# Performance work log

Hardware: AMD Instinct MI355X
Metric: run time of the kernel (lower is better)

## Reference

```python
import jax, jax.numpy as jnp
import numpy as np

NDIM = 8
P = NDIM * (NDIM - 1) // 2  # 28 upper-triangular pairs
NHIDDEN = 128
NLAYERS = 3  # first layer + (NLAYERS-1) hidden layers, all followed by softplus
BATCH = 65536


def _pair_indices():
    # torch code iterates j outer, i inner, keeping i < j (i >= j skipped)
    pairs = [(i, j) for j in range(NDIM) for i in range(NDIM) if i < j]
    rel = np.array([[k for k in range(NDIM) if k != i and k != j] for (i, j) in pairs],
                   dtype=np.int32)  # [P, NDIM-2]
    i_idx = np.array([p[0] for p in pairs], dtype=np.int32)
    j_idx = np.array([p[1] for p in pairs], dtype=np.int32)
    return rel, i_idx, j_idx


def setup_inputs() -> dict:
    key = jax.random.key(0)
    ks = jax.random.split(key, 7)
    rel, i_idx, j_idx = _pair_indices()
    d_in = NDIM - 2
    x = jax.random.normal(ks[0], (BATCH, NDIM), dtype=jnp.float32)
    # stacked per-pair MLP parameters (kaiming-ish scale)
    W1 = jax.random.normal(ks[1], (P, d_in, NHIDDEN), dtype=jnp.float32) / np.sqrt(d_in)
    b1 = jax.random.normal(ks[2], (P, NHIDDEN), dtype=jnp.float32) * 0.05
    Wh = jax.random.normal(ks[3], (NLAYERS - 1, P, NHIDDEN, NHIDDEN), dtype=jnp.float32) / np.sqrt(NHIDDEN)
    bh = jax.random.normal(ks[4], (NLAYERS - 1, P, NHIDDEN), dtype=jnp.float32) * 0.05
    Wout = jax.random.normal(ks[5], (P, NHIDDEN), dtype=jnp.float32) / np.sqrt(NHIDDEN)
    bout = jax.random.normal(ks[6], (P,), dtype=jnp.float32) * 0.05
    return {
        "x": x, "W1": W1, "b1": b1, "Wh": Wh, "bh": bh,
        "Wout": Wout, "bout": bout,
        "rel_idx": jnp.asarray(rel), "i_idx": jnp.asarray(i_idx), "j_idx": jnp.asarray(j_idx),
    }


def reference(x, W1, b1, Wh, bh, Wout, bout, rel_idx, i_idx, j_idx):
    # gather the ndim-2 relevant coords for every pair: [B, P, NDIM-2]
    xg = x[:, rel_idx]
    # first linear + softplus (batched over the P pairs)
    h = jax.nn.softplus(jnp.einsum('bpd,pdh->bph', xg, W1) + b1)
    # hidden linears + softplus
    for l in range(Wh.shape[0]):
        h = jax.nn.softplus(jnp.einsum('bph,phk->bpk', h, Wh[l]) + bh[l])
    # output head (no activation): scalar per pair -> [B, P]
    vals = jnp.einsum('bph,ph->bp', h, Wout) + bout
    # scatter into upper triangle, then antisymmetrize
    B = x.shape[0]
    J = jnp.zeros((B, NDIM, NDIM), dtype=x.dtype).at[:, i_idx, j_idx].set(vals)
    return J - jnp.swapaxes(J, 1, 2)
```

## Files before the change

### kernel.cpp

```cpp
#include <hip/hip_runtime.h>

#define NDIM 8
#define P_PAIRS 28
#define HID 128
#define BATCH_N 65536
#define TILE_M 256
#define THREADS 1024
#define TILES_PER_BLOCK 4

#define LOG2E 1.4426950408889634f
#define LN2   0.6931471805599453f

typedef __attribute__((ext_vector_type(8))) short bf16x8;
typedef __attribute__((ext_vector_type(4))) float f32x4;

#define MEM_FENCE asm volatile("" ::: "memory")

__device__ __forceinline__ unsigned short f32_to_bf16(float f) {
  union { float f; unsigned u; } v; v.f = f;
  unsigned r = v.u + 0x7FFFu + ((v.u >> 16) & 1u);
  return (unsigned short)(r >> 16);
}

__device__ __forceinline__ unsigned cvt_pk_bf16(float a, float b) {
  unsigned r;
  asm("v_cvt_pk_bf16_f32 %0, %1, %2" : "=v"(r) : "v"(a), "v"(b));
  return r;
}

__device__ __forceinline__ float fast_exp2(float x) {
  float r; asm("v_exp_f32 %0, %1" : "=v"(r) : "v"(x)); return r;
}
__device__ __forceinline__ float fast_log2(float x) {
  float r; asm("v_log_f32 %0, %1" : "=v"(r) : "v"(x)); return r;
}

__device__ __forceinline__ float softplus2(float t) {
  t = fminf(t, 30.0f);
  return fast_log2(1.0f + fast_exp2(t));
}

__device__ __forceinline__ int swz(int r, int c8) {
  return r * 128 + (((c8 ^ (r & 15)) & 15) << 3);
}

__global__ void prep_wt(const float* __restrict__ Wh, unsigned short* __restrict__ WT) {
  __shared__ float tile[32][33];
  int t = blockIdx.x;
  int lp = t >> 4;
  int sub = t & 15;
  int kt = (sub >> 2) * 32, nt = (sub & 3) * 32;
  const float* src = Wh + (size_t)lp * 16384;
  unsigned short* dst = WT + (size_t)lp * 16384;
  int tx = threadIdx.x & 31, ty = threadIdx.x >> 5;
#pragma unroll
  for (int r = 0; r < 32; r += 8)
    tile[r + ty][tx] = src[(kt + r + ty) * 128 + (nt + tx)];
  __syncthreads();
#pragma unroll
  for (int r = 0; r < 32; r += 8)
    dst[(nt + r + ty) * 128 + (kt + tx)] = f32_to_bf16(tile[tx][r + ty]);
}

__launch_bounds__(THREADS, 4)
__global__ void mlp_pairs(const float* __restrict__ x,
                          const float* __restrict__ W1,
                          const float* __restrict__ b1,
                          const float* __restrict__ bh,
                          const float* __restrict__ Wout,
                          const float* __restrict__ bout,
                          const int* __restrict__ rel_idx,
                          const int* __restrict__ i_idx,
                          const int* __restrict__ j_idx,
                          const unsigned short* __restrict__ WT,
                          float* __restrict__ out) {
  const int p = blockIdx.y;
  const int bx = blockIdx.x;
  const int tid = (int)threadIdx.x;
  const int lane = tid & 63;
  const int wave = tid >> 6;
  const int qd = lane >> 4;
  const int ln = lane & 15;
  const int mrow = wave * 16;

  __shared__ __align__(16) unsigned short w0_lds[128 * 128];
  __shared__ __align__(16) unsigned short w1_lds[128 * 128];
  __shared__ __align__(16) unsigned short h_lds[TILE_M * 128];
  __shared__ __align__(16) unsigned short w1t_lds[128][8];
  __shared__ __align__(16) float b1s[128];
  __shared__ __align__(16) float bh0s[128];
  __shared__ __align__(16) float bh1s[128];
  __shared__ __align__(16) float wouts[128];

  {
    const uint4* s0 = reinterpret_cast<const uint4*>(WT + (size_t)p * 16384);
    const uint4* s1 = reinterpret_cast<const uint4*>(WT + (size_t)(P_PAIRS + p) * 16384);
#pragma unroll
    for (int it = 0; it < 2; ++it) {
      int idx = it * THREADS + tid;
      int r = idx >> 4, c = idx & 15;
      uint4 a = s0[idx];
      uint4 b = s1[idx];
      int off = swz(r, c);
      *reinterpret_cast<uint4*>(&w0_lds[off]) = a;
      *reinterpret_cast<uint4*>(&w1_lds[off]) = b;
    }
  }
  if (tid < 128) {
    int n = tid;
    unsigned short u[8];
#pragma unroll
    for (int k = 0; k < 6; ++k)
      u[k] = f32_to_bf16(W1[(p * 6 + k) * 128 + n] * LOG2E);
    u[6] = 0; u[7] = 0;
    uint4 pk;
    pk.x = (unsigned)u[0] | ((unsigned)u[1] << 16);
    pk.y = (unsigned)u[2] | ((unsigned)u[3] << 16);
    pk.z = (unsigned)u[4] | ((unsigned)u[5] << 16);
    pk.w = 0u;
    *reinterpret_cast<uint4*>(&w1t_lds[n][0]) = pk;
  } else if (tid < 256) {
    int n = tid - 128;
    b1s[n]  = b1[p * 128 + n] * LOG2E;
    bh0s[n] = bh[p * 128 + n] * LOG2E;
    bh1s[n] = bh[(P_PAIRS + p) * 128 + n] * LOG2E;
    wouts[n] = Wout[p * 128 + n] * LN2;
  }
  int rl[6];
#pragma unroll
  for (int d = 0; d < 6; ++d) rl[d] = rel_idx[p * 6 + d];
  const int ii = i_idx[p], jj = j_idx[p];
  const float bp = bout[p];
  __syncthreads();

  const int phase = ((wave >> 2) & 1) * 2;

  const int ln3 = ln & 3;
  const int rdx = ((qd ^ ln3) << 3) + ((ln >> 2) << 5);
  const int a0  = ln * 128 + rdx;
  const int b0  = (mrow + ln) * 128 + rdx;
  const int hw0 = (mrow + ln) * 128 + (((qd >> 1) ^ (ln & 1)) << 3)
                + (((ln >> 1) & 7) << 4) + (qd & 1) * 4;

  float4 xa = {0.f, 0.f, 0.f, 0.f}, xb = {0.f, 0.f, 0.f, 0.f};
  {
    int row = bx * (TILE_M * TILES_PER_BLOCK) + phase * TILE_M + mrow + ln;
    const float4* xr = reinterpret_cast<const float4*>(x + (size_t)row * 8);
    if (lane < 16) { xa = xr[0]; xb = xr[1]; }
  }

  for (int s = 0; s < TILES_PER_BLOCK; ++s) {
    const int itile = (s + phase) & 3;
    const int row0 = bx * (TILE_M * TILES_PER_BLOCK) + itile * TILE_M;

    bf16x8 zero8 = {};
    bf16x8 bfr1 = zero8;
    if (lane < 16) {
      float xv[8] = {xa.x, xa.y, xa.z, xa.w, xb.x, xb.y, xb.z, xb.w};
      uint4 pk;
      pk.x = cvt_pk_bf16(xv[rl[0]], xv[rl[1]]);
      pk.y = cvt_pk_bf16(xv[rl[2]], xv[rl[3]]);
      pk.z = cvt_pk_bf16(xv[rl[4]], xv[rl[5]]);
      pk.w = 0u;
      bfr1 = __builtin_bit_cast(bf16x8, pk);
    }
    if (s + 1 < TILES_PER_BLOCK && lane < 16) {
      int nrow0 = bx * (TILE_M * TILES_PER_BLOCK) + (((s + 1 + phase) & 3)) * TILE_M;
      const float4* xr = reinterpret_cast<const float4*>(x + (size_t)(nrow0 + mrow + ln) * 8);
      xa = xr[0]; xb = xr[1];
    }

    f32x4 acc[8];

    {
#pragma unroll
      for (int nt = 0; nt < 8; ++nt) {
        bf16x8 afr = zero8;
        if (qd == 0)
          afr = *reinterpret_cast<const bf16x8*>(&w1t_lds[nt * 16 + ln][0]);
        f32x4 b4 = *reinterpret_cast<const f32x4*>(&b1s[nt * 16 + qd * 4]);
        acc[nt] = __builtin_amdgcn_mfma_f32_16x16x32_bf16(afr, bfr1, b4, 0, 0, 0);
      }
    }
#pragma unroll
    for (int nt = 0; nt < 8; ++nt) {
      uint2 pk;
      pk.x = cvt_pk_bf16(softplus2(acc[nt][0]), softplus2(acc[nt][1]));
      pk.y = cvt_pk_bf16(softplus2(acc[nt][2]), softplus2(acc[nt][3]));
      *reinterpret_cast<uint2*>(&h_lds[hw0 ^ (nt << 4)]) = pk;
    }
    MEM_FENCE;

    {
      bf16x8 bfr = *reinterpret_cast<const bf16x8*>(&h_lds[b0]);
#pragma unroll
      for (int nt = 0; nt < 8; ++nt) {
        bf16x8 afr = *reinterpret_cast<const bf16x8*>(&w0_lds[a0 + nt * 2048]);
        f32x4 b4 = *reinterpret_cast<const f32x4*>(&bh0s[nt * 16 + qd * 4]);
        acc[nt] = __builtin_amdgcn_mfma_f32_16x16x32_bf16(afr, bfr, b4, 0, 0, 0);
      }
    }
#pragma unroll
    for (int ks = 1; ks < 4; ++ks) {
      bf16x8 bfr = *reinterpret_cast<const bf16x8*>(&h_lds[b0 ^ (ks << 5)]);
      bf16x8 afr[8];
#pragma unroll
      for (int nt = 0; nt < 8; ++nt)
        afr[nt] = *reinterpret_cast<const bf16x8*>(&w0_lds[(a0 ^ (ks << 5)) + nt * 2048]);
#pragma unroll
      for (int nt = 0; nt < 8; ++nt)
        acc[nt] = __builtin_amdgcn_mfma_f32_16x16x32_bf16(afr[nt], bfr, acc[nt], 0, 0, 0);
    }
#pragma unroll
    for (int nt = 0; nt < 8; ++nt) {
      uint2 pk;
      pk.x = cvt_pk_bf16(softplus2(acc[nt][0]), softplus2(acc[nt][1]));
      pk.y = cvt_pk_bf16(softplus2(acc[nt][2]), softplus2(acc[nt][3]));
      *reinterpret_cast<uint2*>(&h_lds[hw0 ^ (nt << 4)]) = pk;
    }
    MEM_FENCE;

    {
      bf16x8 bfr = *reinterpret_cast<const bf16x8*>(&h_lds[b0]);
#pragma unroll
      for (int nt = 0; nt < 8; ++nt) {
        bf16x8 afr = *reinterpret_cast<const bf16x8*>(&w1_lds[a0 + nt * 2048]);
        f32x4 b4 = *reinterpret_cast<const f32x4*>(&bh1s[nt * 16 + qd * 4]);
        acc[nt] = __builtin_amdgcn_mfma_f32_16x16x32_bf16(afr, bfr, b4, 0, 0, 0);
      }
    }
#pragma unroll
    for (int ks = 1; ks < 4; ++ks) {
      bf16x8 bfr = *reinterpret_cast<const bf16x8*>(&h_lds[b0 ^ (ks << 5)]);
      bf16x8 afr[8];
#pragma unroll
      for (int nt = 0; nt < 8; ++nt)
        afr[nt] = *reinterpret_cast<const bf16x8*>(&w1_lds[(a0 ^ (ks << 5)) + nt * 2048]);
#pragma unroll
      for (int nt = 0; nt < 8; ++nt)
        acc[nt] = __builtin_amdgcn_mfma_f32_16x16x32_bf16(afr[nt], bfr, acc[nt], 0, 0, 0);
    }
    float pv = 0.f;
#pragma unroll
    for (int nt = 0; nt < 8; ++nt) {
      f32x4 wo4 = *reinterpret_cast<const f32x4*>(&wouts[nt * 16 + qd * 4]);
#pragma unroll
      for (int r = 0; r < 4; ++r)
        pv += wo4[r] * softplus2(acc[nt][r]);
    }

    {
      float v = pv;
      v += __shfl_xor(v, 16, 64);
      v += __shfl_xor(v, 32, 64);
      if (lane < 16) {
        int mg = row0 + mrow + lane;
        float val = v + bp;
        out[mg * 64 + ii * 8 + jj] = val;
        out[mg * 64 + jj * 8 + ii] = -val;
        if (p == 0) {
#pragma unroll
          for (int d = 0; d < 8; ++d)
            out[mg * 64 + d * 9] = 0.f;
        }
      }
    }
    MEM_FENCE;
  }
}

extern "C" void kernel_launch(void* const* d_in, const int* in_sizes, int n_in,
                              void* d_out, int out_size, void* d_ws, size_t ws_size,
                              hipStream_t stream) {
  const float* x    = (const float*)d_in[0];
  const float* W1   = (const float*)d_in[1];
  const float* b1   = (const float*)d_in[2];
  const float* Wh   = (const float*)d_in[3];
  const float* bh   = (const float*)d_in[4];
  const float* Wout = (const float*)d_in[5];
  const float* bout = (const float*)d_in[6];
  const int* rel    = (const int*)d_in[7];
  const int* iidx   = (const int*)d_in[8];
  const int* jidx   = (const int*)d_in[9];
  float* out = (float*)d_out;
  unsigned short* WT = (unsigned short*)d_ws;

  prep_wt<<<dim3(56 * 16), 256, 0, stream>>>(Wh, WT);
  dim3 grid(BATCH_N / (TILE_M * TILES_PER_BLOCK), P_PAIRS);
  mlp_pairs<<<grid, THREADS, 0, stream>>>(x, W1, b1, bh, Wout, bout, rel, iidx, jidx, WT, out);
}
```

Before: 307.4 us.

## Replace softplus log with polynomial, fold pair gather into zero-padded W1, hoist Wout

```diff
diff --git a/kernel.cpp b/kernel.cpp
--- a/kernel.cpp
+++ b/kernel.cpp
@@ -31,13 +31,18 @@
 __device__ __forceinline__ float fast_exp2(float x) {
   float r; asm("v_exp_f32 %0, %1" : "=v"(r) : "v"(x)); return r;
 }
-__device__ __forceinline__ float fast_log2(float x) {
-  float r; asm("v_log_f32 %0, %1" : "=v"(r) : "v"(x)); return r;
-}
 
 __device__ __forceinline__ float softplus2(float t) {
-  t = fminf(t, 30.0f);
-  return fast_log2(1.0f + fast_exp2(t));
+  float m = fminf(t, -t);
+  float u = fast_exp2(m);
+  u = fminf(u, 1.0f);
+  float r = fminf(fmaxf(t, 0.0f), 30.0f);
+  float p = fmaf(0.0439283f, u, -0.1898270f);
+  p = fmaf(p, u, 0.4115527f);
+  p = fmaf(p, u, -0.7072470f);
+  p = fmaf(p, u, 1.4416005f);
+  p = fmaf(p, u, 5.713e-5f);
+  return r + p;
 }
 
 __device__ __forceinline__ int swz(int r, int c8) {
@@ -106,18 +111,23 @@
       *reinterpret_cast<uint4*>(&w1_lds[off]) = b;
     }
   }
+  const int ii = i_idx[p], jj = j_idx[p];
   if (tid < 128) {
     int n = tid;
     unsigned short u[8];
 #pragma unroll
-    for (int k = 0; k < 6; ++k)
-      u[k] = f32_to_bf16(W1[(p * 6 + k) * 128 + n] * LOG2E);
-    u[6] = 0; u[7] = 0;
+    for (int k = 0; k < 8; ++k) {
+      bool skip = (k == ii) || (k == jj);
+      int d = k - (k > ii) - (k > jj);
+      if (skip) d = 0;
+      float w = skip ? 0.f : W1[(p * 6 + d) * 128 + n] * LOG2E;
+      u[k] = f32_to_bf16(w);
+    }
     uint4 pk;
     pk.x = (unsigned)u[0] | ((unsigned)u[1] << 16);
     pk.y = (unsigned)u[2] | ((unsigned)u[3] << 16);
     pk.z = (unsigned)u[4] | ((unsigned)u[5] << 16);
-    pk.w = 0u;
+    pk.w = (unsigned)u[6] | ((unsigned)u[7] << 16);
     *reinterpret_cast<uint4*>(&w1t_lds[n][0]) = pk;
   } else if (tid < 256) {
     int n = tid - 128;
@@ -126,14 +136,10 @@
     bh1s[n] = bh[(P_PAIRS + p) * 128 + n] * LOG2E;
     wouts[n] = Wout[p * 128 + n] * LN2;
   }
-  int rl[6];
-#pragma unroll
-  for (int d = 0; d < 6; ++d) rl[d] = rel_idx[p * 6 + d];
-  const int ii = i_idx[p], jj = j_idx[p];
   const float bp = bout[p];
   __syncthreads();
 
-  const int phase = ((wave >> 2) & 1) * 2;
+  const int phase = wave >> 2;
 
   const int ln3 = ln & 3;
   const int rdx = ((qd ^ ln3) << 3) + ((ln >> 2) << 5);
@@ -142,6 +148,11 @@
   const int hw0 = (mrow + ln) * 128 + (((qd >> 1) ^ (ln & 1)) << 3)
                 + (((ln >> 1) & 7) << 4) + (qd & 1) * 4;
 
+  f32x4 wreg[8];
+#pragma unroll
+  for (int nt = 0; nt < 8; ++nt)
+    wreg[nt] = *reinterpret_cast<const f32x4*>(&wouts[nt * 16 + qd * 4]);
+
   float4 xa = {0.f, 0.f, 0.f, 0.f}, xb = {0.f, 0.f, 0.f, 0.f};
   {
     int row = bx * (TILE_M * TILES_PER_BLOCK) + phase * TILE_M + mrow + ln;
@@ -156,12 +167,11 @@
     bf16x8 zero8 = {};
     bf16x8 bfr1 = zero8;
     if (lane < 16) {
-      float xv[8] = {xa.x, xa.y, xa.z, xa.w, xb.x, xb.y, xb.z, xb.w};
       uint4 pk;
-      pk.x = cvt_pk_bf16(xv[rl[0]], xv[rl[1]]);
-      pk.y = cvt_pk_bf16(xv[rl[2]], xv[rl[3]]);
-      pk.z = cvt_pk_bf16(xv[rl[4]], xv[rl[5]]);
-      pk.w = 0u;
+      pk.x = cvt_pk_bf16(xa.x, xa.y);
+      pk.y = cvt_pk_bf16(xa.z, xa.w);
+      pk.z = cvt_pk_bf16(xb.x, xb.y);
+      pk.w = cvt_pk_bf16(xb.z, xb.w);
       bfr1 = __builtin_bit_cast(bf16x8, pk);
     }
     if (s + 1 < TILES_PER_BLOCK && lane < 16) {
@@ -243,10 +253,9 @@
     float pv = 0.f;
 #pragma unroll
     for (int nt = 0; nt < 8; ++nt) {
-      f32x4 wo4 = *reinterpret_cast<const f32x4*>(&wouts[nt * 16 + qd * 4]);
 #pragma unroll
       for (int r = 0; r < 4; ++r)
-        pv += wo4[r] * softplus2(acc[nt][r]);
+        pv += wreg[nt][r] * softplus2(acc[nt][r]);
     }
 
     {
```

Result: slower. 384.7 us (+25.1%).
